# Optimization experiments

Hardware: AMD Instinct MI355X
Metric: run time of the kernel (lower is better)

## Reference

```python
import jax, jax.numpy as jnp
import numpy as np

H = 16  # num_heads
THETA = 10000.0


def apply_rope(x, positions, theta=THETA):
    # x: [..., S, d_k]; positions: [S]
    d_k = x.shape[-1]
    inv_freq = theta ** (-jnp.arange(0, d_k, 2, dtype=jnp.float32) / d_k)  # [d_k/2]
    ang = positions.astype(jnp.float32)[:, None] * inv_freq[None, :]  # [S, d_k/2]
    cos, sin = jnp.cos(ang), jnp.sin(ang)
    x1 = x[..., 0::2]
    x2 = x[..., 1::2]
    out_even = x1 * cos - x2 * sin
    out_odd = x1 * sin + x2 * cos
    out = jnp.stack([out_even, out_odd], axis=-1)  # [..., S, d_k/2, 2]
    return out.reshape(x.shape)


def setup_inputs() -> dict:
    key = jax.random.key(0)
    k1, k2, k3 = jax.random.split(key, 3)
    B, S, D = 2, 2048, 1024
    x = jax.random.normal(k1, (B, S, D), dtype=jnp.float32)
    token_positions = jnp.arange(S, dtype=jnp.int32)
    w_qkv = jax.random.normal(k2, (3 * D, D), dtype=jnp.float32) * (D ** -0.5)
    w_out = jax.random.normal(k3, (D, D), dtype=jnp.float32) * (D ** -0.5)
    return {"x": x, "token_positions": token_positions, "w_qkv": w_qkv, "w_out": w_out}


def reference(x, token_positions, w_qkv, w_out):
    B, S, D = x.shape
    d_k = D // H
    qkv = jnp.einsum('bsd,ed->bse', x, w_qkv)  # [B,S,3D]
    # split '(n h d_k)' -> n=3, h=H, d_k
    qkv = qkv.reshape(B, S, 3, H, d_k).transpose(2, 0, 3, 1, 4)  # [3,B,H,S,d_k]
    q = apply_rope(qkv[0], token_positions)
    k = apply_rope(qkv[1], token_positions)
    v = qkv[2]
    scale = 1.0 / jnp.sqrt(jnp.asarray(d_k, dtype=x.dtype))
    scores = jnp.einsum('bhqd,bhkd->bhqk', q, k) * scale  # [B,H,S,S]
    causal = jnp.tril(jnp.ones((S, S), dtype=bool))
    scores = jnp.where(causal, scores, jnp.asarray(-1e30, dtype=scores.dtype))
    attn = jax.nn.softmax(scores, axis=-1)
    out = jnp.einsum('bhqk,bhkd->bhqd', attn, v)  # [B,H,S,d_k]
    out = out.transpose(0, 2, 1, 3).reshape(B, S, D)  # merge (h d_v)
    return jnp.einsum('bsd,ed->bse', out, w_out)
```

## Files before the change

kernel.cpp:

```cpp
#include <hip/hip_runtime.h>

using bf16 = __bf16;
typedef __bf16 bf16x2 __attribute__((ext_vector_type(2)));
typedef __bf16 bf16x4v __attribute__((ext_vector_type(4)));
typedef __bf16 bf16x8 __attribute__((ext_vector_type(8)));
typedef float f32x4 __attribute__((ext_vector_type(4)));
typedef float floatx4 __attribute__((ext_vector_type(4)));

#define MFMA16(a, b, c) __builtin_amdgcn_mfma_f32_16x16x32_bf16((a), (b), (c), 0, 0, 0)

__device__ __forceinline__ float exp2a(float x) {
  float r;
  asm("v_exp_f32 %0, %1" : "=v"(r) : "v"(x));
  return r;
}

__global__ __launch_bounds__(256) void cast3_kernel(const float* __restrict__ a,
                                                    const float* __restrict__ b,
                                                    const float* __restrict__ c,
                                                    bf16* __restrict__ oa,
                                                    bf16* __restrict__ ob,
                                                    bf16* __restrict__ oc) {
  int i = blockIdx.x * 256 + threadIdx.x;
  const float* in;
  bf16* out;
  int off;
  if (i < 1048576) {
    in = a; out = oa; off = i;
  } else if (i < 1835008) {
    in = b; out = ob; off = i - 1048576;
  } else {
    in = c; out = oc; off = i - 1835008;
  }
  floatx4 v = *(const floatx4*)(in + (size_t)off * 4);
  bf16x4v o;
  #pragma unroll
  for (int j = 0; j < 4; ++j) o[j] = (bf16)v[j];
  *(bf16x4v*)(out + (size_t)off * 4) = o;
}

template <bool OUT_F32, bool ROPE>
__global__ __launch_bounds__(256, 2) void gemm_bt(const bf16* __restrict__ A,
                                                  const bf16* __restrict__ B,
                                                  void* __restrict__ Cv,
                                                  int M, int N, int K,
                                                  const int* __restrict__ pos) {
  __shared__ bf16 As[128 * 32];
  __shared__ bf16 Bs[128 * 32];
  const int t = threadIdx.x;
  const int l = t & 63;
  const int w = t >> 6;
  const int m0 = blockIdx.y * 128;
  const int n0 = blockIdx.x * 128;
  const int wr = (w >> 1) * 64;
  const int wc = (w & 1) * 64;
  const int lr = l & 15;
  const int lk = (l >> 4) * 8;

  f32x4 acc[4][4] = {};

  const int srow = t >> 2;
  const int scol = (t & 3) * 8;

  for (int k0 = 0; k0 < K; k0 += 32) {
    __syncthreads();
    #pragma unroll
    for (int j = 0; j < 2; ++j) {
      const bf16* ga = A + (size_t)(m0 + j * 64 + srow) * K + k0 + scol;
      __builtin_amdgcn_global_load_lds(
          (const __attribute__((address_space(1))) void*)ga,
          (__attribute__((address_space(3))) void*)(As + (j * 64 + srow) * 32 + scol),
          16, 0, 0);
      const bf16* gb = B + (size_t)(n0 + j * 64 + srow) * K + k0 + scol;
      __builtin_amdgcn_global_load_lds(
          (const __attribute__((address_space(1))) void*)gb,
          (__attribute__((address_space(3))) void*)(Bs + (j * 64 + srow) * 32 + scol),
          16, 0, 0);
    }
    __syncthreads();
    bf16x8 af[4], bfr[4];
    #pragma unroll
    for (int i = 0; i < 4; ++i) af[i] = *(const bf16x8*)(As + (wr + i * 16 + lr) * 32 + lk);
    #pragma unroll
    for (int i = 0; i < 4; ++i) bfr[i] = *(const bf16x8*)(Bs + (wc + i * 16 + lr) * 32 + lk);
    #pragma unroll
    for (int i = 0; i < 4; ++i)
      #pragma unroll
      for (int j = 0; j < 4; ++j)
        acc[i][j] = MFMA16(af[i], bfr[j], acc[i][j]);
  }

  const int cr0 = (l >> 4) * 4;
  const int cc = l & 15;

  if constexpr (ROPE) {
    if (n0 < 2048) {
      const float L2T32 = 13.287712379549449f / 32.0f;
      const float INV2PI = 0.15915494309189535f;
      float frev[4];
      #pragma unroll
      for (int j = 0; j < 4; ++j) {
        int col = n0 + wc + j * 16 + cc;
        int ip = (col & 63) >> 1;
        frev[j] = exp2f(-(float)ip * L2T32) * INV2PI;
      }
      const float sgn = (cc & 1) ? 1.f : -1.f;
      #pragma unroll
      for (int i = 0; i < 4; ++i) {
        #pragma unroll
        for (int r = 0; r < 4; ++r) {
          int row = m0 + wr + i * 16 + cr0 + r;
          float p = (float)pos[row & 2047];
          #pragma unroll
          for (int j = 0; j < 4; ++j) {
            float self = acc[i][j][r];
            float partner = __shfl_xor(self, 1, 64);
            float ang = p * frev[j];
            float fr = ang - floorf(ang);
            float sn, cs;
            asm("v_sin_f32 %0, %1" : "=v"(sn) : "v"(fr));
            asm("v_cos_f32 %0, %1" : "=v"(cs) : "v"(fr));
            acc[i][j][r] = self * cs + sgn * sn * partner;
          }
        }
      }
    }
  }

  #pragma unroll
  for (int i = 0; i < 4; ++i) {
    #pragma unroll
    for (int j = 0; j < 4; ++j) {
      int row = m0 + wr + i * 16 + cr0;
      int col = n0 + wc + j * 16 + cc;
      #pragma unroll
      for (int r = 0; r < 4; ++r) {
        if constexpr (OUT_F32)
          ((float*)Cv)[(size_t)(row + r) * N + col] = acc[i][j][r];
        else
          ((bf16*)Cv)[(size_t)(row + r) * N + col] = (bf16)acc[i][j][r];
      }
    }
  }
}

__global__ __launch_bounds__(256, 4) void fa_causal(const bf16* __restrict__ qkv,
                                                    bf16* __restrict__ attn) {
  const int bh = blockIdx.x;
  const int b = bh >> 4, h = bh & 15;
  const int q0 = ((int)gridDim.y - 1 - (int)blockIdx.y) * 64;
  const int t = threadIdx.x, w = t >> 6, l = t & 63;
  const int lq = l & 15;
  const int g = l >> 4;
  const int lk = g * 8;
  const int swz = lq & 7;
  const int hz = lq >> 3;

  __shared__ bf16 Ks[2][64 * 64];
  __shared__ bf16 Vt[2][64 * 64];

  const size_t rs = 3072;
  const bf16* Qg = qkv + (size_t)(b * 2048) * rs + h * 64;
  const bf16* Kg = Qg + 1024;
  const bf16* Vg = Qg + 2048;

  const int qrow0 = q0 + w * 16;
  const int qg = qrow0 + lq;

  const float SC = 0.125f * 1.44269504088896f;
  bf16x8 qfr[2];
  #pragma unroll
  for (int kk = 0; kk < 2; ++kk) {
    bf16x8 qv = *(const bf16x8*)(Qg + (size_t)qg * rs + kk * 32 + lk);
    #pragma unroll
    for (int j = 0; j < 8; ++j) qv[j] = (bf16)((float)qv[j] * SC);
    qfr[kk] = qv;
  }

  f32x4 o[4] = {};
  float mrow = -1e30f, lrow = 0.f;

  const int nkt = (q0 + 64) >> 6;
  const int krow_in = l >> 3;
  const int kcsrc = (l & 7) ^ krow_in;
  const int kp = t >> 3;
  const int K0 = kp * 2;
  const int cd = t & 7;
  const int slot0 = (K0 & 32) | (((K0 >> 2) & 3) << 3) | (((K0 >> 4) & 1) << 2) | (K0 & 3);

  bf16x8 va, vb2;

  #define STAGE_K(KT, BUF)                                                                \
    {                                                                                     \
      _Pragma("unroll")                                                                   \
      for (int c = 0; c < 2; ++c) {                                                       \
        const int rowbase = w * 8 + c * 32;                                               \
        const bf16* src = Kg + (size_t)((KT)*64 + rowbase + krow_in) * rs + kcsrc * 8;    \
        __builtin_amdgcn_global_load_lds(                                                 \
            (const __attribute__((address_space(1))) void*)src,                           \
            (__attribute__((address_space(3))) void*)(&Ks[BUF][rowbase * 64]), 16, 0, 0); \
      }                                                                                   \
    }
  #define LOAD_V(KT)                                                          \
    {                                                                         \
      const bf16* vsrc = Vg + (size_t)((KT)*64 + K0) * rs + cd * 8;           \
      va = *(const bf16x8*)(vsrc);                                            \
      vb2 = *(const bf16x8*)(vsrc + rs);                                      \
    }
  #define WRITE_V(BUF)                                                        \
    {                                                                         \
      _Pragma("unroll")                                                       \
      for (int e = 0; e < 8; ++e) {                                           \
        bf16x2 pr;                                                            \
        pr[0] = va[e];                                                        \
        pr[1] = vb2[e];                                                       \
        *(bf16x2*)(&Vt[BUF][(cd * 8 + e) * 64 + (slot0 ^ ((e ^ cd) << 3))]) = pr; \
      }                                                                       \
    }

  STAGE_K(0, 0)
  LOAD_V(0)
  WRITE_V(0)
  __syncthreads();

  for (int kt = 0; kt < nkt; ++kt) {
    const bool pf = (kt + 1 < nkt);
    if (pf) {
      LOAD_V(kt + 1)
      STAGE_K(kt + 1, (kt + 1) & 1)
    }

    if (kt * 64 <= qrow0 + 15) {
      const bf16* Kc = Ks[kt & 1];
      const bf16* Vc = Vt[kt & 1];
      const bool fullw = (kt * 64 + 63 <= qrow0);

      f32x4 sc[4] = {};
      __builtin_amdgcn_s_setprio(1);
      #pragma unroll
      for (int kf = 0; kf < 4; ++kf) {
        const int krow = kf * 16 + lq;
        bf16x8 kb0 = *(const bf16x8*)(&Kc[krow * 64 + ((0 + g) ^ swz) * 8]);
        bf16x8 kb1 = *(const bf16x8*)(&Kc[krow * 64 + ((4 + g) ^ swz) * 8]);
        sc[kf] = MFMA16(kb0, qfr[0], sc[kf]);
        sc[kf] = MFMA16(kb1, qfr[1], sc[kf]);
      }
      __builtin_amdgcn_s_setprio(0);

      float pv[16];
      if (fullw) {
        #pragma unroll
        for (int i = 0; i < 16; ++i) pv[i] = sc[i >> 2][i & 3];
      } else {
        #pragma unroll
        for (int kf = 0; kf < 4; ++kf)
          #pragma unroll
          for (int r = 0; r < 4; ++r) {
            int key = kt * 64 + kf * 16 + g * 4 + r;
            pv[kf * 4 + r] = (key <= qg) ? sc[kf][r] : -1e30f;
          }
      }
      float mxl = fmaxf(fmaxf(pv[0], pv[1]), pv[2]);
      mxl = fmaxf(fmaxf(mxl, pv[3]), pv[4]);
      mxl = fmaxf(fmaxf(mxl, pv[5]), pv[6]);
      mxl = fmaxf(fmaxf(mxl, pv[7]), pv[8]);
      mxl = fmaxf(fmaxf(mxl, pv[9]), pv[10]);
      mxl = fmaxf(fmaxf(mxl, pv[11]), pv[12]);
      mxl = fmaxf(fmaxf(mxl, pv[13]), pv[14]);
      mxl = fmaxf(mxl, pv[15]);
      if (!__all(mxl <= mrow)) {
        float mx = fmaxf(mxl, __shfl_xor(mxl, 16, 64));
        mx = fmaxf(mx, __shfl_xor(mx, 32, 64));
        float mnew = fmaxf(mrow, mx);
        float al = exp2a(mrow - mnew);
        lrow *= al;
        #pragma unroll
        for (int fd = 0; fd < 4; ++fd)
          #pragma unroll
          for (int r = 0; r < 4; ++r) o[fd][r] *= al;
        mrow = mnew;
      }
      float rsum = 0.f;
      #pragma unroll
      for (int i = 0; i < 16; ++i) {
        float p = exp2a(pv[i] - mrow);
        pv[i] = p;
        rsum += p;
      }
      rsum += __shfl_xor(rsum, 16, 64);
      rsum += __shfl_xor(rsum, 32, 64);
      lrow += rsum;

      bf16x8 p0, p1;
      #pragma unroll
      for (int i = 0; i < 8; ++i) {
        p0[i] = (bf16)pv[i];
        p1[i] = (bf16)pv[8 + i];
      }

      __builtin_amdgcn_s_setprio(1);
      #pragma unroll
      for (int fd = 0; fd < 4; ++fd) {
        const int drow = fd * 16 + lq;
        {
          int pc = (0 * 4 + g) ^ swz ^ (fd << 1) ^ hz;
          bf16x8 vb = *(const bf16x8*)(&Vc[drow * 64 + pc * 8]);
          o[fd] = MFMA16(vb, p0, o[fd]);
        }
        {
          int pc = (1 * 4 + g) ^ swz ^ (fd << 1) ^ hz;
          bf16x8 vb = *(const bf16x8*)(&Vc[drow * 64 + pc * 8]);
          o[fd] = MFMA16(vb, p1, o[fd]);
        }
      }
      __builtin_amdgcn_s_setprio(0);
    }

    if (pf) {
      WRITE_V((kt + 1) & 1)
      __syncthreads();
    }
  }

  __syncthreads();
  bf16* Os = (bf16*)Ks + w * (16 * 72);
  float inv = 1.0f / lrow;
  #pragma unroll
  for (int fd = 0; fd < 4; ++fd) {
    bf16x4v ov;
    #pragma unroll
    for (int r = 0; r < 4; ++r) ov[r] = (bf16)(o[fd][r] * inv);
    *(bf16x4v*)(&Os[lq * 72 + fd * 16 + g * 4]) = ov;
  }
  asm volatile("" ::: "memory");
  #pragma unroll
  for (int p = 0; p < 2; ++p) {
    int idx = p * 64 + l;
    int row16 = idx >> 3, c8 = idx & 7;
    bf16x8 v = *(const bf16x8*)(&Os[row16 * 72 + c8 * 8]);
    *(bf16x8*)(&attn[(size_t)(b * 2048 + qrow0 + row16) * 1024 + h * 64 + c8 * 8]) = v;
  }
}

extern "C" void kernel_launch(void* const* d_in, const int* in_sizes, int n_in,
                              void* d_out, int out_size, void* d_ws, size_t ws_size,
                              hipStream_t stream) {
  const float* x = (const float*)d_in[0];
  const int* pos = (const int*)d_in[1];
  const float* w_qkv = (const float*)d_in[2];
  const float* w_out = (const float*)d_in[3];
  float* out = (float*)d_out;

  char* ws = (char*)d_ws;
  bf16* xb   = (bf16*)(ws);
  bf16* wqb  = (bf16*)(ws + (8u << 20));
  bf16* wob  = (bf16*)(ws + (14u << 20));
  bf16* qkv  = (bf16*)(ws + (16u << 20));
  bf16* attn = (bf16*)(ws + (40u << 20));

  cast3_kernel<<<8192, 256, 0, stream>>>(x, w_qkv, w_out, xb, wqb, wob);

  dim3 g1(3072 / 128, 4096 / 128);
  gemm_bt<false, true><<<g1, 256, 0, stream>>>(xb, wqb, (void*)qkv, 4096, 3072, 1024, pos);

  dim3 gfa(32, 2048 / 64);
  fa_causal<<<gfa, 256, 0, stream>>>(qkv, attn);

  dim3 g2(1024 / 128, 4096 / 128);
  gemm_bt<true, false><<<g2, 256, 0, stream>>>(attn, wob, (void*)out, 4096, 1024, 1024, nullptr);
}
```

Baseline: 114.6 us.

## Precompute RoPE sin/cos table and widen attention blocks to 128 queries

RoPE cos/sin values are now computed once into a table inside the cast kernel, and the QKV GEMM epilogue reads that table instead of evaluating transcendentals per element. The attention kernel moves to 512 threads covering 128 query rows per block, so each K/V tile staged in shared memory serves twice as many queries, and the per-thread K/V load work is split accordingly. The row max and row sum reductions become tree-shaped to shorten dependency chains. The table reuses the attn workspace region, which is safe only because the QKV GEMM finishes reading it before attention overwrites it. The larger blocks halve the number of attention blocks and may lower occupancy.

```diff
diff --git a/kernel.cpp b/kernel.cpp
--- a/kernel.cpp
+++ b/kernel.cpp
@@ -20,8 +20,18 @@
                                                     const float* __restrict__ c,
                                                     bf16* __restrict__ oa,
                                                     bf16* __restrict__ ob,
-                                                    bf16* __restrict__ oc) {
+                                                    bf16* __restrict__ oc,
+                                                    const int* __restrict__ pos,
+                                                    float2* __restrict__ tab) {
   int i = blockIdx.x * 256 + threadIdx.x;
+  if (i < 65536) {
+    int s = i >> 5, ip = i & 31;
+    float freq = exp2f(-(float)ip * (13.287712379549449f / 32.0f));
+    float ang = (float)pos[s] * freq;
+    float sn, cs;
+    sincosf(ang, &sn, &cs);
+    tab[i] = make_float2(cs, sn);
+  }
   const float* in;
   bf16* out;
   int off;
@@ -44,7 +54,7 @@
                                                   const bf16* __restrict__ B,
                                                   void* __restrict__ Cv,
                                                   int M, int N, int K,
-                                                  const int* __restrict__ pos) {
+                                                  const float2* __restrict__ tab) {
   __shared__ bf16 As[128 * 32];
   __shared__ bf16 Bs[128 * 32];
   const int t = threadIdx.x;
@@ -95,32 +105,22 @@
 
   if constexpr (ROPE) {
     if (n0 < 2048) {
-      const float L2T32 = 13.287712379549449f / 32.0f;
-      const float INV2PI = 0.15915494309189535f;
-      float frev[4];
-      #pragma unroll
-      for (int j = 0; j < 4; ++j) {
-        int col = n0 + wc + j * 16 + cc;
-        int ip = (col & 63) >> 1;
-        frev[j] = exp2f(-(float)ip * L2T32) * INV2PI;
-      }
+      int ip[4];
+      #pragma unroll
+      for (int j = 0; j < 4; ++j) ip[j] = ((n0 + wc + j * 16 + cc) & 63) >> 1;
       const float sgn = (cc & 1) ? 1.f : -1.f;
       #pragma unroll
       for (int i = 0; i < 4; ++i) {
         #pragma unroll
         for (int r = 0; r < 4; ++r) {
           int row = m0 + wr + i * 16 + cr0 + r;
-          float p = (float)pos[row & 2047];
+          int s = row & 2047;
           #pragma unroll
           for (int j = 0; j < 4; ++j) {
+            float2 cs = tab[s * 32 + ip[j]];
             float self = acc[i][j][r];
             float partner = __shfl_xor(self, 1, 64);
-            float ang = p * frev[j];
-            float fr = ang - floorf(ang);
-            float sn, cs;
-            asm("v_sin_f32 %0, %1" : "=v"(sn) : "v"(fr));
-            asm("v_cos_f32 %0, %1" : "=v"(cs) : "v"(fr));
-            acc[i][j][r] = self * cs + sgn * sn * partner;
+            acc[i][j][r] = self * cs.x + sgn * cs.y * partner;
           }
         }
       }
@@ -144,11 +144,11 @@
   }
 }
 
-__global__ __launch_bounds__(256, 4) void fa_causal(const bf16* __restrict__ qkv,
+__global__ __launch_bounds__(512, 4) void fa_causal(const bf16* __restrict__ qkv,
                                                     bf16* __restrict__ attn) {
   const int bh = blockIdx.x;
   const int b = bh >> 4, h = bh & 15;
-  const int q0 = ((int)gridDim.y - 1 - (int)blockIdx.y) * 64;
+  const int q0 = ((int)gridDim.y - 1 - (int)blockIdx.y) * 128;
   const int t = threadIdx.x, w = t >> 6, l = t & 63;
   const int lq = l & 15;
   const int g = l >> 4;
@@ -156,8 +156,7 @@
   const int swz = lq & 7;
   const int hz = lq >> 3;
 
-  __shared__ bf16 Ks[2][64 * 64];
-  __shared__ bf16 Vt[2][64 * 64];
+  __shared__ bf16 SH[4][64 * 64];
 
   const size_t rs = 3072;
   const bf16* Qg = qkv + (size_t)(b * 2048) * rs + h * 64;
@@ -180,42 +179,40 @@
   f32x4 o[4] = {};
   float mrow = -1e30f, lrow = 0.f;
 
-  const int nkt = (q0 + 64) >> 6;
+  const int nkt = (q0 + 128) >> 6;
   const int krow_in = l >> 3;
   const int kcsrc = (l & 7) ^ krow_in;
-  const int kp = t >> 3;
+  const int kp = t >> 4;
   const int K0 = kp * 2;
+  const int sub = (t >> 3) & 1;
   const int cd = t & 7;
   const int slot0 = (K0 & 32) | (((K0 >> 2) & 3) << 3) | (((K0 >> 4) & 1) << 2) | (K0 & 3);
 
-  bf16x8 va, vb2;
-
-  #define STAGE_K(KT, BUF)                                                                \
-    {                                                                                     \
-      _Pragma("unroll")                                                                   \
-      for (int c = 0; c < 2; ++c) {                                                       \
-        const int rowbase = w * 8 + c * 32;                                               \
-        const bf16* src = Kg + (size_t)((KT)*64 + rowbase + krow_in) * rs + kcsrc * 8;    \
-        __builtin_amdgcn_global_load_lds(                                                 \
-            (const __attribute__((address_space(1))) void*)src,                           \
-            (__attribute__((address_space(3))) void*)(&Ks[BUF][rowbase * 64]), 16, 0, 0); \
-      }                                                                                   \
-    }
-  #define LOAD_V(KT)                                                          \
-    {                                                                         \
-      const bf16* vsrc = Vg + (size_t)((KT)*64 + K0) * rs + cd * 8;           \
-      va = *(const bf16x8*)(vsrc);                                            \
-      vb2 = *(const bf16x8*)(vsrc + rs);                                      \
-    }
-  #define WRITE_V(BUF)                                                        \
-    {                                                                         \
-      _Pragma("unroll")                                                       \
-      for (int e = 0; e < 8; ++e) {                                           \
-        bf16x2 pr;                                                            \
-        pr[0] = va[e];                                                        \
-        pr[1] = vb2[e];                                                       \
-        *(bf16x2*)(&Vt[BUF][(cd * 8 + e) * 64 + (slot0 ^ ((e ^ cd) << 3))]) = pr; \
-      }                                                                       \
+  bf16x4v va4, vb4;
+
+  #define STAGE_K(KT, BUF)                                                              \
+    {                                                                                   \
+      const bf16* src = Kg + (size_t)((KT)*64 + w * 8 + krow_in) * rs + kcsrc * 8;      \
+      __builtin_amdgcn_global_load_lds(                                                 \
+          (const __attribute__((address_space(1))) void*)src,                           \
+          (__attribute__((address_space(3))) void*)(&SH[BUF][(w * 8) * 64]), 16, 0, 0); \
+    }
+  #define LOAD_V(KT)                                                                   \
+    {                                                                                  \
+      const bf16* vsrc = Vg + (size_t)((KT)*64 + K0) * rs + cd * 8 + sub * 4;          \
+      va4 = *(const bf16x4v*)(vsrc);                                                   \
+      vb4 = *(const bf16x4v*)(vsrc + rs);                                              \
+    }
+  #define WRITE_V(BUF)                                                                 \
+    {                                                                                  \
+      _Pragma("unroll")                                                                \
+      for (int j = 0; j < 4; ++j) {                                                    \
+        int e = sub * 4 + j;                                                           \
+        bf16x2 pr;                                                                     \
+        pr[0] = va4[j];                                                                \
+        pr[1] = vb4[j];                                                                \
+        *(bf16x2*)(&SH[2 + (BUF)][(cd * 8 + e) * 64 + (slot0 ^ ((e ^ cd) << 3))]) = pr; \
+      }                                                                                \
     }
 
   STAGE_K(0, 0)
@@ -231,8 +228,8 @@
     }
 
     if (kt * 64 <= qrow0 + 15) {
-      const bf16* Kc = Ks[kt & 1];
-      const bf16* Vc = Vt[kt & 1];
+      const bf16* Kc = SH[kt & 1];
+      const bf16* Vc = SH[2 + (kt & 1)];
       const bool fullw = (kt * 64 + 63 <= qrow0);
 
       f32x4 sc[4] = {};
@@ -260,14 +257,13 @@
             pv[kf * 4 + r] = (key <= qg) ? sc[kf][r] : -1e30f;
           }
       }
-      float mxl = fmaxf(fmaxf(pv[0], pv[1]), pv[2]);
-      mxl = fmaxf(fmaxf(mxl, pv[3]), pv[4]);
-      mxl = fmaxf(fmaxf(mxl, pv[5]), pv[6]);
-      mxl = fmaxf(fmaxf(mxl, pv[7]), pv[8]);
-      mxl = fmaxf(fmaxf(mxl, pv[9]), pv[10]);
-      mxl = fmaxf(fmaxf(mxl, pv[11]), pv[12]);
-      mxl = fmaxf(fmaxf(mxl, pv[13]), pv[14]);
-      mxl = fmaxf(mxl, pv[15]);
+      float m0_ = fmaxf(pv[0], pv[1]), m1_ = fmaxf(pv[2], pv[3]);
+      float m2_ = fmaxf(pv[4], pv[5]), m3_ = fmaxf(pv[6], pv[7]);
+      float m4_ = fmaxf(pv[8], pv[9]), m5_ = fmaxf(pv[10], pv[11]);
+      float m6_ = fmaxf(pv[12], pv[13]), m7_ = fmaxf(pv[14], pv[15]);
+      float ma = fmaxf(fmaxf(m0_, m1_), fmaxf(m2_, m3_));
+      float mb = fmaxf(fmaxf(m4_, m5_), fmaxf(m6_, m7_));
+      float mxl = fmaxf(ma, mb);
       if (!__all(mxl <= mrow)) {
         float mx = fmaxf(mxl, __shfl_xor(mxl, 16, 64));
         mx = fmaxf(mx, __shfl_xor(mx, 32, 64));
@@ -280,13 +276,13 @@
           for (int r = 0; r < 4; ++r) o[fd][r] *= al;
         mrow = mnew;
       }
-      float rsum = 0.f;
-      #pragma unroll
-      for (int i = 0; i < 16; ++i) {
-        float p = exp2a(pv[i] - mrow);
-        pv[i] = p;
-        rsum += p;
-      }
+      #pragma unroll
+      for (int i = 0; i < 16; ++i) pv[i] = exp2a(pv[i] - mrow);
+      float s0_ = pv[0] + pv[1], s1_ = pv[2] + pv[3];
+      float s2_ = pv[4] + pv[5], s3_ = pv[6] + pv[7];
+      float s4_ = pv[8] + pv[9], s5_ = pv[10] + pv[11];
+      float s6_ = pv[12] + pv[13], s7_ = pv[14] + pv[15];
+      float rsum = ((s0_ + s1_) + (s2_ + s3_)) + ((s4_ + s5_) + (s6_ + s7_));
       rsum += __shfl_xor(rsum, 16, 64);
       rsum += __shfl_xor(rsum, 32, 64);
       lrow += rsum;
@@ -323,7 +319,7 @@
   }
 
   __syncthreads();
-  bf16* Os = (bf16*)Ks + w * (16 * 72);
+  bf16* Os = (bf16*)SH + w * (16 * 72);
   float inv = 1.0f / lrow;
   #pragma unroll
   for (int fd = 0; fd < 4; ++fd) {
@@ -357,14 +353,15 @@
   bf16* wob  = (bf16*)(ws + (14u << 20));
   bf16* qkv  = (bf16*)(ws + (16u << 20));
   bf16* attn = (bf16*)(ws + (40u << 20));
-
-  cast3_kernel<<<8192, 256, 0, stream>>>(x, w_qkv, w_out, xb, wqb, wob);
+  float2* tab = (float2*)(ws + (40u << 20));
+
+  cast3_kernel<<<8192, 256, 0, stream>>>(x, w_qkv, w_out, xb, wqb, wob, pos, tab);
 
   dim3 g1(3072 / 128, 4096 / 128);
-  gemm_bt<false, true><<<g1, 256, 0, stream>>>(xb, wqb, (void*)qkv, 4096, 3072, 1024, pos);
-
-  dim3 gfa(32, 2048 / 64);
-  fa_causal<<<gfa, 256, 0, stream>>>(qkv, attn);
+  gemm_bt<false, true><<<g1, 256, 0, stream>>>(xb, wqb, (void*)qkv, 4096, 3072, 1024, tab);
+
+  dim3 gfa(32, 2048 / 128);
+  fa_causal<<<gfa, 512, 0, stream>>>(qkv, attn);
 
   dim3 g2(1024 / 128, 4096 / 128);
   gemm_bt<true, false><<<g2, 256, 0, stream>>>(attn, wob, (void*)out, 4096, 1024, 1024, nullptr);
```

After: 115.0 us. No clear change (+0.4%).
